# Optimization experiments

Measured on AMD Instinct MI355X. Metric: run time of the kernel, lower is better.

Reference implementation:

```python
import jax, jax.numpy as jnp
import numpy as np

N = 20000      # total nodes (100 graphs x 200 nodes)
B = 100        # batch_size
PER = 200      # nodes per graph (uniform) -> max_num_nodes
E = 320000     # edges (before self-loops)
F_IN = 32      # num_features
HEADS = 10
OUT = 128      # output_dim
NEG_SLOPE = 0.2  # PyG GATConv default


def setup_inputs() -> dict:
    key = jax.random.key(0)
    ks = jax.random.split(key, 14)
    feats = jax.random.normal(ks[0], (N, F_IN), jnp.float32)
    src = jax.random.randint(ks[1], (E,), 0, N)
    dst = jax.random.randint(ks[2], (E,), 0, N)
    edge_index = jnp.stack([src, dst]).astype(jnp.int32)
    graph_id = jnp.repeat(jnp.arange(B, dtype=jnp.int32), PER)
    batch_num_nodes = jnp.full((B,), PER, jnp.int32)
    s1 = 1.0 / np.sqrt(F_IN)
    s2 = 1.0 / np.sqrt(F_IN * HEADS)
    s3 = 1.0 / np.sqrt(OUT)
    return {
        "feats": feats,
        "edge_index": edge_index,
        "graph_id": graph_id,
        "batch_num_nodes": batch_num_nodes,
        # GATConv 1: in F_IN -> HEADS x F_IN, concat
        "W1": jax.random.normal(ks[3], (F_IN, HEADS * F_IN), jnp.float32) * s1,
        "a1_src": jax.random.normal(ks[4], (HEADS, F_IN), jnp.float32) * s1,
        "a1_dst": jax.random.normal(ks[5], (HEADS, F_IN), jnp.float32) * s1,
        "b1": jnp.zeros((HEADS * F_IN,), jnp.float32),
        "W2": jax.random.normal(ks[6], (HEADS * F_IN, OUT), jnp.float32) * s2,
        "a2_src": jax.random.normal(ks[7], (1, OUT), jnp.float32) * s3,
        "a2_dst": jax.random.normal(ks[8], (1, OUT), jnp.float32) * s3,
        "b2": jnp.zeros((OUT,), jnp.float32),
        # shared fc_g1
        "fc_w": jax.random.normal(ks[9], (OUT, OUT), jnp.float32) * s3,
        "fc_b": jnp.zeros((OUT,), jnp.float32),
    }


def gat_conv(x, src, dst, W, a_src, a_dst, bias, heads, out_dim):
    # x: [N, Fin]; src/dst already include self-loops (PyG default add_self_loops=True)
    n = x.shape[0]
    xw = (x @ W).reshape(n, heads, out_dim)                 # [N,H,F]
    s_src = jnp.einsum('nhf,hf->nh', xw, a_src)             # [N,H]
    s_dst = jnp.einsum('nhf,hf->nh', xw, a_dst)
    e = jax.nn.leaky_relu(s_src[src] + s_dst[dst], NEG_SLOPE)  # [E,H]
    # segment softmax over incoming edges of each destination node
    m = jax.ops.segment_max(e, dst, num_segments=n)         # [N,H]
    ex = jnp.exp(e - m[dst])
    denom = jax.ops.segment_sum(ex, dst, num_segments=n)    # [N,H]
    alpha = ex / jnp.maximum(denom[dst], 1e-16)             # [E,H]
    out = jax.ops.segment_sum(alpha[:, :, None] * xw[src], dst, num_segments=n)  # [N,H,F]
    return out.reshape(n, heads * out_dim) + bias


def reference(feats, edge_index, graph_id, batch_num_nodes,
              W1, a1_src, a1_dst, b1, W2, a2_src, a2_dst, b2, fc_w, fc_b):
    n = feats.shape[0]
    loops = jnp.arange(n, dtype=edge_index.dtype)
    src = jnp.concatenate([edge_index[0], loops])
    dst = jnp.concatenate([edge_index[1], loops])
    x = feats.astype(jnp.float32)
    # dropout layers are identity in eval mode
    x = jax.nn.elu(gat_conv(x, src, dst, W1, a1_src, a1_dst, b1, HEADS, F_IN))
    x = gat_conv(x, src, dst, W2, a2_src, a2_dst, b2, 1, OUT)
    x = jax.nn.relu(x)                                       # [N, OUT]
    # dgl_split: scatter node feats into [B, max_num_nodes, OUT] padded tensor
    cum = jnp.concatenate([jnp.zeros((1,), jnp.int32),
                           jnp.cumsum(batch_num_nodes).astype(jnp.int32)])
    idx = jnp.arange(n, dtype=jnp.int32) - cum[graph_id] + graph_id * PER
    padded = jnp.zeros((B * PER, OUT), x.dtype).at[idx].set(x).reshape(B, PER, OUT)
    out = jax.nn.relu(padded @ fc_w + fc_b)                  # [B, PER, OUT]
    # global max pool per graph, then shared fc_g1 + relu
    pooled = jax.ops.segment_max(x, graph_id, num_segments=B)  # [B, OUT]
    pooled = jax.nn.relu(pooled @ fc_w + fc_b)
    return (out, pooled)
```

## Files before the change

kernel.cpp:

```cpp
#include <hip/hip_runtime.h>

#define N_NODES 20000
#define N_EDGES 320000
#define ETOT    (N_EDGES + N_NODES)
#define HEADS   10
#define F_IN    32
#define C1      (HEADS * F_IN)
#define C2      128
#define NB      100
#define PER     200
#define CAP     96
#define HSTRIDE 328
#define X2STRIDE 136

typedef __attribute__((ext_vector_type(8))) short bf16x8;
typedef __attribute__((ext_vector_type(4))) float floatx4;
typedef _Float16 f16;
typedef _Float16 f16x2 __attribute__((ext_vector_type(2)));
typedef _Float16 f16x8 __attribute__((ext_vector_type(8)));

static __device__ __forceinline__ unsigned short f2bf(float f) {
    unsigned int u = __float_as_uint(f);
    unsigned int r = (u + 0x7fffu + ((u >> 16) & 1u)) >> 16;
    return (unsigned short)r;
}

#define CURZ_BLOCKS ((N_NODES + 255) / 256)
#define PLZ_BLOCKS  ((NB * C2 + 255) / 256)
#define W2P_BLOCKS  ((C1 * C2 + 255) / 256)
#define W1P_BLOCKS  ((HEADS * F_IN * F_IN + 255) / 256)
#define FCP_BLOCKS  ((C2 * C2 + 255) / 256)
#define F16_BLOCKS  ((N_NODES * F_IN / 4 + 255) / 256)
__global__ void prep_kernel(int* __restrict__ cursor, int* __restrict__ pooledi,
                            const float* __restrict__ W2, unsigned short* __restrict__ W2p,
                            const float* __restrict__ W1, unsigned short* __restrict__ W1p,
                            const float* __restrict__ fcw, f16* __restrict__ FCp,
                            const float* __restrict__ a1s, const float* __restrict__ a1d,
                            float* __restrict__ WAs, float* __restrict__ WAd,
                            const float* __restrict__ feats, f16* __restrict__ feats16) {
    unsigned int b = blockIdx.x;
    if (b < CURZ_BLOCKS) {
        int o = b * 256 + threadIdx.x;
        if (o < N_NODES) cursor[o] = 0;
        return;
    }
    b -= CURZ_BLOCKS;
    if (b < PLZ_BLOCKS) {
        int o = b * 256 + threadIdx.x;
        if (o < NB * C2) pooledi[o] = 0;
        return;
    }
    b -= PLZ_BLOCKS;
    if (b < W2P_BLOCKS) {
        int o = b * 256 + threadIdx.x;
        if (o >= C1 * C2) return;
        int j    = o & 7;
        int lane = (o >> 3) & 63;
        int ct   = (o >> 9) & 7;
        int kb   = o >> 12;
        int k = kb * 32 + (lane >> 4) * 8 + j;
        int n = ct * 16 + (lane & 15);
        W2p[o] = f2bf(W2[k * C2 + n]);
        return;
    }
    b -= W2P_BLOCKS;
    if (b < W1P_BLOCKS) {
        int o = b * 256 + threadIdx.x;
        if (o >= HEADS * F_IN * F_IN) return;
        int j    = o & 7;
        int lane = (o >> 3) & 63;
        int ct   = (o >> 9) & 1;
        int h    = o >> 10;
        int k = (lane >> 4) * 8 + j;
        int f = ct * 16 + (lane & 15);
        W1p[o] = f2bf(W1[k * C1 + h * 32 + f]);
        return;
    }
    b -= W1P_BLOCKS;
    if (b < FCP_BLOCKS) {
        int o = b * 256 + threadIdx.x;
        if (o >= C2 * C2) return;
        int j    = o & 7;
        int lane = (o >> 3) & 63;
        int ct   = (o >> 9) & 7;
        int kb   = o >> 12;
        int k = kb * 32 + (lane >> 4) * 8 + j;
        int n = ct * 16 + (lane & 15);
        FCp[o] = (f16)fcw[k * C2 + n];
        return;
    }
    b -= FCP_BLOCKS;
    if (b < F16_BLOCKS) {
        int o = b * 256 + threadIdx.x;
        if (o < N_NODES * F_IN / 4) {
            float4 v = ((const float4*)feats)[o];
            f16* d = feats16 + 4 * o;
            d[0] = (f16)v.x; d[1] = (f16)v.y; d[2] = (f16)v.z; d[3] = (f16)v.w;
        }
        return;
    }
    int t = threadIdx.x;
    for (int o = t; o < C1; o += 256) {
        int k = o & 31, h = o >> 5;
        float ss = 0.f, dd = 0.f;
#pragma unroll
        for (int f = 0; f < F_IN; f++) {
            float wv = W1[k * C1 + h * 32 + f];
            ss += wv * a1s[h * 32 + f];
            dd += wv * a1d[h * 32 + f];
        }
        WAs[k * HEADS + h] = ss;
        WAd[k * HEADS + h] = dd;
    }
}

#define SCAT_BLOCKS ((ETOT + 255) / 256)
__global__ __launch_bounds__(256) void scatter_score_kernel(
        const int* __restrict__ ei, int* __restrict__ cursor, int* __restrict__ csr_src,
        const float* __restrict__ feats, const float* __restrict__ WAs,
        const float* __restrict__ WAd, float* __restrict__ s_src,
        float* __restrict__ s_dst) {
    if (blockIdx.x < SCAT_BLOCKS) {
        int e = blockIdx.x * 256 + threadIdx.x;
        if (e >= ETOT) return;
        int s, d;
        if (e < N_EDGES) { s = ei[e]; d = ei[N_EDGES + e]; }
        else             { s = e - N_EDGES; d = s; }
        int pos = atomicAdd(&cursor[d], 1);
        csr_src[(size_t)d * CAP + pos] = s;
        return;
    }
    __shared__ __align__(16) float A[64 * F_IN];
    __shared__ float Ws[C1], Wd[C1];
    int t = threadIdx.x;
    int n0 = (blockIdx.x - SCAT_BLOCKS) * 64;
    int nrows = min(64, N_NODES - n0);
    if (nrows <= 0) return;
    for (int i = t; i < C1; i += 256) { Ws[i] = WAs[i]; Wd[i] = WAd[i]; }
    const float4* fs = (const float4*)(feats + (size_t)n0 * F_IN);
    float4* Af = (float4*)A;
    for (int i = t; i < nrows * 8; i += 256) Af[i] = fs[i];
    __syncthreads();
    for (int o = t; o < nrows * HEADS; o += 256) {
        int nl = o / HEADS, h = o - nl * HEADS;
        const float* ar = A + nl * F_IN;
        float ss = 0.f, dd = 0.f;
#pragma unroll
        for (int k = 0; k < F_IN; k++) {
            float av = ar[k];
            ss += av * Ws[k * HEADS + h];
            dd += av * Wd[k * HEADS + h];
        }
        s_src[(size_t)(n0 + nl) * HEADS + h] = ss;
        s_dst[(size_t)(n0 + nl) * HEADS + h] = dd;
    }
}

__global__ __launch_bounds__(256) void aggg1_kernel(
        const f16* __restrict__ feats16, const float* __restrict__ s_src,
        const float* __restrict__ s_dst, const int* __restrict__ deg_arr,
        const int* __restrict__ csr_src, unsigned short* __restrict__ gn) {
    __shared__ __align__(4) f16 shP[4][HEADS * 64];
    __shared__ __align__(8) int shS[4][64];
    int wslot = threadIdx.x >> 6;
    int n = blockIdx.x * 4 + wslot;
    int lane = threadIdx.x & 63;
    int k = lane & 31, half = lane >> 5;
    f16* P = shP[wslot];
    int* S = shS[wslot];
    const f16x2 ones = {(f16)1.f, (f16)1.f};

    int beg = n * CAP, deg = deg_arr[n];
    const float* sdp = s_dst + (size_t)n * HEADS;
    float sd[10];
#pragma unroll
    for (int q = 0; q < 5; q++) {
        float2 v = *(const float2*)(sdp + 2 * q);
        sd[2 * q] = v.x; sd[2 * q + 1] = v.y;
    }
    float g[10], la[10];
#pragma unroll
    for (int h = 0; h < 10; h++) { g[h] = 0.f; la[h] = 0.f; }

    for (int c0 = 0; c0 < deg; c0 += 64) {
        int dc = min(deg - c0, 64);
        bool act = lane < dc;
        int s_e = csr_src[beg + c0 + min(lane, dc - 1)];
        const float* ssp = s_src + (size_t)s_e * HEADS;
        float p[10];
#pragma unroll
        for (int q = 0; q < 5; q++) {
            float2 v = *(const float2*)(ssp + 2 * q);
            float e0 = v.x + sd[2 * q];
            float e1 = v.y + sd[2 * q + 1];
            e0 = (e0 >= 0.f) ? e0 : 0.2f * e0;
            e1 = (e1 >= 0.f) ? e1 : 0.2f * e1;
            p[2 * q]     = act ? __expf(e0) : 0.f;
            p[2 * q + 1] = act ? __expf(e1) : 0.f;
        }
        S[lane] = s_e;
#pragma unroll
        for (int h = 0; h < 10; h++) P[h * 64 + lane] = (f16)p[h];
        asm volatile("s_waitcnt lgkmcnt(0)" ::: "memory");

        int dcp = (dc + 3) & ~3;
        for (int i = 0; i < dcp; i += 4) {
            int e0 = i + half * 2;
            int2 ss2 = *(const int2*)&S[e0];
            f16x2 v;
            v.x = feats16[(size_t)ss2.x * F_IN + k];
            v.y = feats16[(size_t)ss2.y * F_IN + k];
#pragma unroll
            for (int h = 0; h < 10; h++) {
                f16x2 pp = *(const f16x2*)&P[h * 64 + e0];
                g[h]  = __builtin_amdgcn_fdot2(pp, v, g[h], false);
                la[h] = __builtin_amdgcn_fdot2(pp, ones, la[h], false);
            }
        }
        asm volatile("s_waitcnt lgkmcnt(0)" ::: "memory");
    }
#pragma unroll
    for (int h = 0; h < 10; h++) {
        g[h]  += __shfl_xor(g[h], 32);
        la[h] += __shfl_xor(la[h], 32);
    }
    if (half == 0) {
        unsigned short* gp = gn + (size_t)n * C1 + k;
#pragma unroll
        for (int h = 0; h < 10; h++)
            gp[h * 32] = f2bf(g[h] / fmaxf(la[h], 1e-16f));
    }
}

__global__ __launch_bounds__(256) void h1gemm2_kernel(
        const unsigned short* __restrict__ gn, const unsigned short* __restrict__ W1p,
        const float* __restrict__ b1, const unsigned short* __restrict__ W2p,
        const float* __restrict__ a_src, const float* __restrict__ a_dst,
        f16* __restrict__ xw2h, float* __restrict__ s_src2, float* __restrict__ s_dst2) {
    __shared__ unsigned short H[2][16 * HSTRIDE];
    __shared__ float redS[2][2][16], redD[2][2][16];
    int waveId = threadIdx.x >> 6;
    int tl = waveId >> 1;
    int w  = waveId & 1;
    int tile = blockIdx.x * 2 + tl;
    int lane = threadIdx.x & 63;
    int quad = lane >> 4, col = lane & 15;
    int row0 = tile * 16;

#pragma unroll
    for (int hh = 0; hh < 5; hh++) {
        int h = w * 5 + hh;
        bf16x8 a = *(const bf16x8*)(gn + (size_t)(row0 + col) * C1 + h * 32 + quad * 8);
        bf16x8 bA = ((const bf16x8*)W1p)[(h * 2 + 0) * 64 + lane];
        bf16x8 bB = ((const bf16x8*)W1p)[(h * 2 + 1) * 64 + lane];
        floatx4 z = {0.f, 0.f, 0.f, 0.f};
        floatx4 c0 = __builtin_amdgcn_mfma_f32_16x16x32_bf16(a, bA, z, 0, 0, 0);
        floatx4 c1 = __builtin_amdgcn_mfma_f32_16x16x32_bf16(a, bB, z, 0, 0, 0);
        float bias0 = b1[h * 32 + col];
        float bias1 = b1[h * 32 + 16 + col];
#pragma unroll
        for (int reg = 0; reg < 4; reg++) {
            int r = quad * 4 + reg;
            float o0 = c0[reg] + bias0;
            float o1 = c1[reg] + bias1;
            o0 = (o0 > 0.f) ? o0 : (__expf(o0) - 1.f);
            o1 = (o1 > 0.f) ? o1 : (__expf(o1) - 1.f);
            H[tl][r * HSTRIDE + h * 32 + col]      = f2bf(o0);
            H[tl][r * HSTRIDE + h * 32 + 16 + col] = f2bf(o1);
        }
    }
    __syncthreads();

    floatx4 acc[4];
#pragma unroll
    for (int c = 0; c < 4; c++) acc[c] = (floatx4){0.f, 0.f, 0.f, 0.f};
    const bf16x8* pb = (const bf16x8*)W2p;
#pragma unroll
    for (int kb = 0; kb < 10; kb++) {
        bf16x8 a = *(const bf16x8*)&H[tl][(lane & 15) * HSTRIDE + kb * 32 + quad * 8];
#pragma unroll
        for (int c = 0; c < 4; c++) {
            bf16x8 b = pb[(kb * 8 + (4 * w + c)) * 64 + lane];
            acc[c] = __builtin_amdgcn_mfma_f32_16x16x32_bf16(a, b, acc[c], 0, 0, 0);
        }
    }
    float asv[4], adv[4];
#pragma unroll
    for (int c = 0; c < 4; c++) {
        asv[c] = a_src[(4 * w + c) * 16 + col];
        adv[c] = a_dst[(4 * w + c) * 16 + col];
    }
#pragma unroll
    for (int reg = 0; reg < 4; reg++) {
        int row = row0 + quad * 4 + reg;
        float vs = 0.f, vd = 0.f;
#pragma unroll
        for (int c = 0; c < 4; c++) {
            float v = acc[c][reg];
            xw2h[(size_t)row * C2 + (4 * w + c) * 16 + col] = (f16)v;
            vs += v * asv[c];
            vd += v * adv[c];
        }
#pragma unroll
        for (int off = 8; off >= 1; off >>= 1) {
            vs += __shfl_xor(vs, off);
            vd += __shfl_xor(vd, off);
        }
        if (col == 0) { redS[tl][w][quad * 4 + reg] = vs; redD[tl][w][quad * 4 + reg] = vd; }
    }
    __syncthreads();
    if (w == 0) {
        if (lane < 16)
            s_src2[row0 + lane] = redS[tl][0][lane] + redS[tl][1][lane];
        else if (lane < 32)
            s_dst2[row0 + lane - 16] = redD[tl][0][lane - 16] + redD[tl][1][lane - 16];
    }
}

__global__ __launch_bounds__(256) void agg2fc_kernel(
        const f16* __restrict__ xw2h, const float* __restrict__ s_src2,
        const float* __restrict__ s_dst2, const int* __restrict__ deg_arr,
        const int* __restrict__ csr_src, const float* __restrict__ b2,
        const f16* __restrict__ FCp, const float* __restrict__ fcb,
        float* __restrict__ out, int* __restrict__ pooledi) {
    __shared__ __align__(8) int2 shE[4][64];
    __shared__ __align__(16) f16 X[16 * X2STRIDE];
    int wslot = threadIdx.x >> 6;
    int lane = threadIdx.x & 63;
    int tile = blockIdx.x;
    int row0 = tile * 16;
    int2* E = shE[wslot];

#pragma unroll
    for (int rep = 0; rep < 4; rep++) {
        int r = wslot * 4 + rep;
        int n = row0 + r;
        int beg = n * CAP, deg = deg_arr[n];
        float sd = s_dst2[n];
        float l = 0.f, a0 = 0.f, a1 = 0.f;

        for (int c0 = 0; c0 < deg; c0 += 64) {
            int dc = min(deg - c0, 64);
            bool act = lane < dc;
            int s_e = csr_src[beg + c0 + min(lane, dc - 1)];
            float e = s_src2[s_e] + sd;
            e = (e >= 0.f) ? e : 0.2f * e;
            float p = act ? __expf(e) : 0.f;
            float su = p;
#pragma unroll
            for (int off = 32; off >= 1; off >>= 1) su += __shfl_xor(su, off);
            l += su;

            E[lane] = make_int2(s_e, __float_as_int(p));
            asm volatile("s_waitcnt lgkmcnt(0)" ::: "memory");

            int dcr = (dc + 3) & ~3;
            for (int i = 0; i < dcr; i += 4) {
                int2 e0 = E[i + 0], e1 = E[i + 1], e2 = E[i + 2], e3 = E[i + 3];
                f16x2 v0 = *(const f16x2*)(xw2h + (size_t)e0.x * C2 + 2 * lane);
                f16x2 v1 = *(const f16x2*)(xw2h + (size_t)e1.x * C2 + 2 * lane);
                f16x2 v2 = *(const f16x2*)(xw2h + (size_t)e2.x * C2 + 2 * lane);
                f16x2 v3 = *(const f16x2*)(xw2h + (size_t)e3.x * C2 + 2 * lane);
                float p0 = __int_as_float(e0.y), p1 = __int_as_float(e1.y);
                float p2 = __int_as_float(e2.y), p3 = __int_as_float(e3.y);
                a0 += p0 * (float)v0.x + p1 * (float)v1.x + p2 * (float)v2.x + p3 * (float)v3.x;
                a1 += p0 * (float)v0.y + p1 * (float)v1.y + p2 * (float)v2.y + p3 * (float)v3.y;
            }
            asm volatile("s_waitcnt lgkmcnt(0)" ::: "memory");
        }

        float linv = 1.f / fmaxf(l, 1e-16f);
        float2 bb = *(const float2*)(b2 + 2 * lane);
        f16x2 o;
        o.x = (f16)fmaxf(a0 * linv + bb.x, 0.f);
        o.y = (f16)fmaxf(a1 * linv + bb.y, 0.f);
        *(f16x2*)&X[r * X2STRIDE + 2 * lane] = o;
    }
    __syncthreads();

    int quad = lane >> 4, col = lane & 15;
    floatx4 acc[2];
    acc[0] = (floatx4){0.f, 0.f, 0.f, 0.f};
    acc[1] = (floatx4){0.f, 0.f, 0.f, 0.f};
    const f16x8* pb = (const f16x8*)FCp;
#pragma unroll
    for (int kb = 0; kb < 4; kb++) {
        f16x8 a = *(const f16x8*)&X[(lane & 15) * X2STRIDE + kb * 32 + quad * 8];
#pragma unroll
        for (int c = 0; c < 2; c++) {
            int ct = wslot * 2 + c;
            f16x8 b = pb[(kb * 8 + ct) * 64 + lane];
            acc[c] = __builtin_amdgcn_mfma_f32_16x16x32_f16(a, b, acc[c], 0, 0, 0);
        }
    }
#pragma unroll
    for (int c = 0; c < 2; c++) {
        int ct = wslot * 2 + c;
        float bias = fcb[ct * 16 + col];
#pragma unroll
        for (int reg = 0; reg < 4; reg++) {
            int row = row0 + quad * 4 + reg;
            out[(size_t)row * C2 + ct * 16 + col] = fmaxf(acc[c][reg] + bias, 0.f);
        }
    }

    if (threadIdx.x < C2) {
        int c = threadIdx.x;
        int gA = row0 / PER;
        int gB = (row0 + 15) / PER;
        float mA = 0.f, mB = 0.f;
#pragma unroll
        for (int r = 0; r < 16; r++) {
            float v = (float)X[r * X2STRIDE + c];
            if ((row0 + r) / PER == gA) mA = fmaxf(mA, v);
            else                        mB = fmaxf(mB, v);
        }
        atomicMax(&pooledi[gA * C2 + c], __float_as_int(mA));
        if (gB != gA) atomicMax(&pooledi[gB * C2 + c], __float_as_int(mB));
    }
}

__global__ void poolfc_kernel(const int* __restrict__ pooledi, const float* __restrict__ fcw,
                              const float* __restrict__ fcb, float* __restrict__ outp) {
    __shared__ float mx[C2];
    int g = blockIdx.x, t = threadIdx.x;
    mx[t] = __int_as_float(pooledi[g * C2 + t]);
    __syncthreads();
    float acc = 0.f;
    for (int k = 0; k < C2; k++) acc += mx[k] * fcw[k * C2 + t];
    outp[g * C2 + t] = fmaxf(acc + fcb[t], 0.f);
}

extern "C" void kernel_launch(void* const* d_in, const int* in_sizes, int n_in,
                              void* d_out, int out_size, void* d_ws, size_t ws_size,
                              hipStream_t stream) {
    const float* feats = (const float*)d_in[0];
    const int*   ei    = (const int*)d_in[1];
    const float* W1  = (const float*)d_in[4];
    const float* a1s = (const float*)d_in[5];
    const float* a1d = (const float*)d_in[6];
    const float* b1  = (const float*)d_in[7];
    const float* W2  = (const float*)d_in[8];
    const float* a2s = (const float*)d_in[9];
    const float* a2d = (const float*)d_in[10];
    const float* b2  = (const float*)d_in[11];
    const float* fcw = (const float*)d_in[12];
    const float* fcb = (const float*)d_in[13];

    float* out_main = (float*)d_out;
    float* out_pool = (float*)d_out + (size_t)N_NODES * C2;

    char* p = (char*)d_ws;
    auto alloc = [&](size_t bytes) {
        char* r = p;
        p += (bytes + 255) & ~(size_t)255;
        return r;
    };
    unsigned short* gn   = (unsigned short*)alloc(sizeof(short) * (size_t)N_NODES * C1);
    unsigned short* W2p  = (unsigned short*)alloc(sizeof(short) * C1 * C2);
    unsigned short* W1p  = (unsigned short*)alloc(sizeof(short) * HEADS * F_IN * F_IN);
    f16*   FCp     = (f16*)alloc(sizeof(f16) * C2 * C2);
    f16*   feats16 = (f16*)alloc(sizeof(f16) * (size_t)N_NODES * F_IN);
    f16*   xw2h    = (f16*)alloc(sizeof(f16) * (size_t)N_NODES * C2);
    float* WAs    = (float*)alloc(sizeof(float) * C1);
    float* WAd    = (float*)alloc(sizeof(float) * C1);
    float* s1s    = (float*)alloc(sizeof(float) * N_NODES * HEADS);
    float* s1d    = (float*)alloc(sizeof(float) * N_NODES * HEADS);
    float* s2s    = (float*)alloc(sizeof(float) * N_NODES);
    float* s2d    = (float*)alloc(sizeof(float) * N_NODES);
    int* cursor   = (int*)alloc(sizeof(int) * N_NODES);
    int* pooledi  = (int*)alloc(sizeof(int) * NB * C2);
    int* csr_src  = (int*)alloc(sizeof(int) * N_NODES * CAP);

    prep_kernel<<<CURZ_BLOCKS + PLZ_BLOCKS + W2P_BLOCKS + W1P_BLOCKS + FCP_BLOCKS + F16_BLOCKS + 1,
                  256, 0, stream>>>(
        cursor, pooledi, W2, W2p, W1, W1p, fcw, FCp, a1s, a1d, WAs, WAd, feats, feats16);
    scatter_score_kernel<<<SCAT_BLOCKS + (N_NODES + 63) / 64, 256, 0, stream>>>(
        ei, cursor, csr_src, feats, WAs, WAd, s1s, s1d);

    aggg1_kernel<<<5000, 256, 0, stream>>>(feats16, s1s, s1d, cursor, csr_src, gn);
    h1gemm2_kernel<<<625, 256, 0, stream>>>(gn, W1p, b1, W2p, a2s, a2d, xw2h, s2s, s2d);
    agg2fc_kernel<<<1250, 256, 0, stream>>>(xw2h, s2s, s2d, cursor, csr_src, b2,
                                            FCp, fcb, out_main, pooledi);
    poolfc_kernel<<<NB, C2, 0, stream>>>(pooledi, fcw, fcb, out_pool);
}
```

Measured before the change: 167.3 us.

## Fuse layer-1 aggregation with layer-1 projection and layer-2 GEMM in one kernel

Merges the layer-1 edge aggregation kernel and the following W1/ELU/W2 GEMM kernel into one 512-thread block per 16-node tile. Aggregated features now stay in shared memory instead of making a round trip through a global bf16 buffer, and one launch is removed. The agg2fc kernel also moves to 8 waves per 16-row tile, with each wave owning one 16-column output slice. The cost is lower per-block GEMM parallelism, since waves 0-1 handle two heads while the rest handle one. Larger blocks and higher LDS use per block may also reduce occupancy.

```diff
diff --git a/kernel.cpp b/kernel.cpp
--- a/kernel.cpp
+++ b/kernel.cpp
@@ -156,101 +156,96 @@
     }
 }
 
-__global__ __launch_bounds__(256) void aggg1_kernel(
+__global__ __launch_bounds__(512) void aggh1g2_kernel(
         const f16* __restrict__ feats16, const float* __restrict__ s_src,
         const float* __restrict__ s_dst, const int* __restrict__ deg_arr,
-        const int* __restrict__ csr_src, unsigned short* __restrict__ gn) {
-    __shared__ __align__(4) f16 shP[4][HEADS * 64];
-    __shared__ __align__(8) int shS[4][64];
-    int wslot = threadIdx.x >> 6;
-    int n = blockIdx.x * 4 + wslot;
+        const int* __restrict__ csr_src,
+        const unsigned short* __restrict__ W1p, const float* __restrict__ b1,
+        const unsigned short* __restrict__ W2p,
+        const float* __restrict__ a_src, const float* __restrict__ a_dst,
+        f16* __restrict__ xw2h, float* __restrict__ s_src2, float* __restrict__ s_dst2) {
+    __shared__ __align__(4) f16 shP[8][HEADS * 64];
+    __shared__ __align__(8) int shS[8][64];
+    __shared__ __align__(16) unsigned short GT[16 * HSTRIDE];
+    __shared__ __align__(16) unsigned short H[16 * HSTRIDE];
+    __shared__ float redS[8][16], redD[8][16];
+    int w = threadIdx.x >> 6;
     int lane = threadIdx.x & 63;
     int k = lane & 31, half = lane >> 5;
-    f16* P = shP[wslot];
-    int* S = shS[wslot];
+    int row0 = blockIdx.x * 16;
+    f16* P = shP[w];
+    int* S = shS[w];
     const f16x2 ones = {(f16)1.f, (f16)1.f};
 
-    int beg = n * CAP, deg = deg_arr[n];
-    const float* sdp = s_dst + (size_t)n * HEADS;
-    float sd[10];
-#pragma unroll
-    for (int q = 0; q < 5; q++) {
-        float2 v = *(const float2*)(sdp + 2 * q);
-        sd[2 * q] = v.x; sd[2 * q + 1] = v.y;
-    }
-    float g[10], la[10];
-#pragma unroll
-    for (int h = 0; h < 10; h++) { g[h] = 0.f; la[h] = 0.f; }
-
-    for (int c0 = 0; c0 < deg; c0 += 64) {
-        int dc = min(deg - c0, 64);
-        bool act = lane < dc;
-        int s_e = csr_src[beg + c0 + min(lane, dc - 1)];
-        const float* ssp = s_src + (size_t)s_e * HEADS;
-        float p[10];
+#pragma unroll
+    for (int rep = 0; rep < 2; rep++) {
+        int r = w * 2 + rep;
+        int n = row0 + r;
+        int beg = n * CAP, deg = deg_arr[n];
+        const float* sdp = s_dst + (size_t)n * HEADS;
+        float sd[10];
 #pragma unroll
         for (int q = 0; q < 5; q++) {
-            float2 v = *(const float2*)(ssp + 2 * q);
-            float e0 = v.x + sd[2 * q];
-            float e1 = v.y + sd[2 * q + 1];
-            e0 = (e0 >= 0.f) ? e0 : 0.2f * e0;
-            e1 = (e1 >= 0.f) ? e1 : 0.2f * e1;
-            p[2 * q]     = act ? __expf(e0) : 0.f;
-            p[2 * q + 1] = act ? __expf(e1) : 0.f;
-        }
-        S[lane] = s_e;
-#pragma unroll
-        for (int h = 0; h < 10; h++) P[h * 64 + lane] = (f16)p[h];
-        asm volatile("s_waitcnt lgkmcnt(0)" ::: "memory");
-
-        int dcp = (dc + 3) & ~3;
-        for (int i = 0; i < dcp; i += 4) {
-            int e0 = i + half * 2;
-            int2 ss2 = *(const int2*)&S[e0];
-            f16x2 v;
-            v.x = feats16[(size_t)ss2.x * F_IN + k];
-            v.y = feats16[(size_t)ss2.y * F_IN + k];
-#pragma unroll
-            for (int h = 0; h < 10; h++) {
-                f16x2 pp = *(const f16x2*)&P[h * 64 + e0];
-                g[h]  = __builtin_amdgcn_fdot2(pp, v, g[h], false);
-                la[h] = __builtin_amdgcn_fdot2(pp, ones, la[h], false);
+            float2 v = *(const float2*)(sdp + 2 * q);
+            sd[2 * q] = v.x; sd[2 * q + 1] = v.y;
+        }
+        float g[10], la[10];
+#pragma unroll
+        for (int h = 0; h < 10; h++) { g[h] = 0.f; la[h] = 0.f; }
+
+        for (int c0 = 0; c0 < deg; c0 += 64) {
+            int dc = min(deg - c0, 64);
+            bool act = lane < dc;
+            int s_e = csr_src[beg + c0 + min(lane, dc - 1)];
+            const float* ssp = s_src + (size_t)s_e * HEADS;
+            float p[10];
+#pragma unroll
+            for (int q = 0; q < 5; q++) {
+                float2 v = *(const float2*)(ssp + 2 * q);
+                float e0 = v.x + sd[2 * q];
+                float e1 = v.y + sd[2 * q + 1];
+                e0 = (e0 >= 0.f) ? e0 : 0.2f * e0;
+                e1 = (e1 >= 0.f) ? e1 : 0.2f * e1;
+                p[2 * q]     = act ? __expf(e0) : 0.f;
+                p[2 * q + 1] = act ? __expf(e1) : 0.f;
             }
-        }
-        asm volatile("s_waitcnt lgkmcnt(0)" ::: "memory");
-    }
-#pragma unroll
-    for (int h = 0; h < 10; h++) {
-        g[h]  += __shfl_xor(g[h], 32);
-        la[h] += __shfl_xor(la[h], 32);
-    }
-    if (half == 0) {
-        unsigned short* gp = gn + (size_t)n * C1 + k;
-#pragma unroll
-        for (int h = 0; h < 10; h++)
-            gp[h * 32] = f2bf(g[h] / fmaxf(la[h], 1e-16f));
-    }
-}
-
-__global__ __launch_bounds__(256) void h1gemm2_kernel(
-        const unsigned short* __restrict__ gn, const unsigned short* __restrict__ W1p,
-        const float* __restrict__ b1, const unsigned short* __restrict__ W2p,
-        const float* __restrict__ a_src, const float* __restrict__ a_dst,
-        f16* __restrict__ xw2h, float* __restrict__ s_src2, float* __restrict__ s_dst2) {
-    __shared__ unsigned short H[2][16 * HSTRIDE];
-    __shared__ float redS[2][2][16], redD[2][2][16];
-    int waveId = threadIdx.x >> 6;
-    int tl = waveId >> 1;
-    int w  = waveId & 1;
-    int tile = blockIdx.x * 2 + tl;
-    int lane = threadIdx.x & 63;
+            S[lane] = s_e;
+#pragma unroll
+            for (int h = 0; h < 10; h++) P[h * 64 + lane] = (f16)p[h];
+            asm volatile("s_waitcnt lgkmcnt(0)" ::: "memory");
+
+            int dcp = (dc + 3) & ~3;
+            for (int i = 0; i < dcp; i += 4) {
+                int e0 = i + half * 2;
+                int2 ss2 = *(const int2*)&S[e0];
+                f16x2 v;
+                v.x = feats16[(size_t)ss2.x * F_IN + k];
+                v.y = feats16[(size_t)ss2.y * F_IN + k];
+#pragma unroll
+                for (int h = 0; h < 10; h++) {
+                    f16x2 pp = *(const f16x2*)&P[h * 64 + e0];
+                    g[h]  = __builtin_amdgcn_fdot2(pp, v, g[h], false);
+                    la[h] = __builtin_amdgcn_fdot2(pp, ones, la[h], false);
+                }
+            }
+            asm volatile("s_waitcnt lgkmcnt(0)" ::: "memory");
+        }
+#pragma unroll
+        for (int h = 0; h < 10; h++) {
+            g[h]  += __shfl_xor(g[h], 32);
+            la[h] += __shfl_xor(la[h], 32);
+        }
+        if (half == 0) {
+#pragma unroll
+            for (int h = 0; h < 10; h++)
+                GT[r * HSTRIDE + h * 32 + k] = f2bf(g[h] / fmaxf(la[h], 1e-16f));
+        }
+    }
+    __syncthreads();
+
     int quad = lane >> 4, col = lane & 15;
-    int row0 = tile * 16;
-
-#pragma unroll
-    for (int hh = 0; hh < 5; hh++) {
-        int h = w * 5 + hh;
-        bf16x8 a = *(const bf16x8*)(gn + (size_t)(row0 + col) * C1 + h * 32 + quad * 8);
+    for (int h = w; h < 10; h += 8) {
+        bf16x8 a = *(const bf16x8*)&GT[col * HSTRIDE + h * 32 + quad * 8];
         bf16x8 bA = ((const bf16x8*)W1p)[(h * 2 + 0) * 64 + lane];
         bf16x8 bB = ((const bf16x8*)W1p)[(h * 2 + 1) * 64 + lane];
         floatx4 z = {0.f, 0.f, 0.f, 0.f};
@@ -265,75 +260,60 @@
             float o1 = c1[reg] + bias1;
             o0 = (o0 > 0.f) ? o0 : (__expf(o0) - 1.f);
             o1 = (o1 > 0.f) ? o1 : (__expf(o1) - 1.f);
-            H[tl][r * HSTRIDE + h * 32 + col]      = f2bf(o0);
-            H[tl][r * HSTRIDE + h * 32 + 16 + col] = f2bf(o1);
-        }
-    }
-    __syncthreads();
-
-    floatx4 acc[4];
-#pragma unroll
-    for (int c = 0; c < 4; c++) acc[c] = (floatx4){0.f, 0.f, 0.f, 0.f};
+            H[r * HSTRIDE + h * 32 + col]      = f2bf(o0);
+            H[r * HSTRIDE + h * 32 + 16 + col] = f2bf(o1);
+        }
+    }
+    __syncthreads();
+
+    floatx4 acc = {0.f, 0.f, 0.f, 0.f};
     const bf16x8* pb = (const bf16x8*)W2p;
 #pragma unroll
     for (int kb = 0; kb < 10; kb++) {
-        bf16x8 a = *(const bf16x8*)&H[tl][(lane & 15) * HSTRIDE + kb * 32 + quad * 8];
-#pragma unroll
-        for (int c = 0; c < 4; c++) {
-            bf16x8 b = pb[(kb * 8 + (4 * w + c)) * 64 + lane];
-            acc[c] = __builtin_amdgcn_mfma_f32_16x16x32_bf16(a, b, acc[c], 0, 0, 0);
-        }
-    }
-    float asv[4], adv[4];
-#pragma unroll
-    for (int c = 0; c < 4; c++) {
-        asv[c] = a_src[(4 * w + c) * 16 + col];
-        adv[c] = a_dst[(4 * w + c) * 16 + col];
-    }
+        bf16x8 a = *(const bf16x8*)&H[(lane & 15) * HSTRIDE + kb * 32 + quad * 8];
+        bf16x8 b = pb[(kb * 8 + w) * 64 + lane];
+        acc = __builtin_amdgcn_mfma_f32_16x16x32_bf16(a, b, acc, 0, 0, 0);
+    }
+    float as = a_src[w * 16 + col], ad = a_dst[w * 16 + col];
 #pragma unroll
     for (int reg = 0; reg < 4; reg++) {
         int row = row0 + quad * 4 + reg;
-        float vs = 0.f, vd = 0.f;
-#pragma unroll
-        for (int c = 0; c < 4; c++) {
-            float v = acc[c][reg];
-            xw2h[(size_t)row * C2 + (4 * w + c) * 16 + col] = (f16)v;
-            vs += v * asv[c];
-            vd += v * adv[c];
-        }
+        float v = acc[reg];
+        xw2h[(size_t)row * C2 + w * 16 + col] = (f16)v;
+        float vs = v * as, vd = v * ad;
 #pragma unroll
         for (int off = 8; off >= 1; off >>= 1) {
             vs += __shfl_xor(vs, off);
             vd += __shfl_xor(vd, off);
         }
-        if (col == 0) { redS[tl][w][quad * 4 + reg] = vs; redD[tl][w][quad * 4 + reg] = vd; }
-    }
-    __syncthreads();
-    if (w == 0) {
-        if (lane < 16)
-            s_src2[row0 + lane] = redS[tl][0][lane] + redS[tl][1][lane];
-        else if (lane < 32)
-            s_dst2[row0 + lane - 16] = redD[tl][0][lane - 16] + redD[tl][1][lane - 16];
-    }
-}
-
-__global__ __launch_bounds__(256) void agg2fc_kernel(
+        if (col == 0) { redS[w][quad * 4 + reg] = vs; redD[w][quad * 4 + reg] = vd; }
+    }
+    __syncthreads();
+    if (threadIdx.x < 16) {
+        float s = 0.f, d = 0.f;
+#pragma unroll
+        for (int ww = 0; ww < 8; ww++) { s += redS[ww][threadIdx.x]; d += redD[ww][threadIdx.x]; }
+        s_src2[row0 + threadIdx.x] = s;
+        s_dst2[row0 + threadIdx.x] = d;
+    }
+}
+
+__global__ __launch_bounds__(512) void agg2fc_kernel(
         const f16* __restrict__ xw2h, const float* __restrict__ s_src2,
         const float* __restrict__ s_dst2, const int* __restrict__ deg_arr,
         const int* __restrict__ csr_src, const float* __restrict__ b2,
         const f16* __restrict__ FCp, const float* __restrict__ fcb,
         float* __restrict__ out, int* __restrict__ pooledi) {
-    __shared__ __align__(8) int2 shE[4][64];
+    __shared__ __align__(8) int2 shE[8][64];
     __shared__ __align__(16) f16 X[16 * X2STRIDE];
-    int wslot = threadIdx.x >> 6;
+    int w = threadIdx.x >> 6;
     int lane = threadIdx.x & 63;
-    int tile = blockIdx.x;
-    int row0 = tile * 16;
-    int2* E = shE[wslot];
-
-#pragma unroll
-    for (int rep = 0; rep < 4; rep++) {
-        int r = wslot * 4 + rep;
+    int row0 = blockIdx.x * 16;
+    int2* E = shE[w];
+
+#pragma unroll
+    for (int rep = 0; rep < 2; rep++) {
+        int r = w * 2 + rep;
         int n = row0 + r;
         int beg = n * CAP, deg = deg_arr[n];
         float sd = s_dst2[n];
@@ -379,29 +359,19 @@
     __syncthreads();
 
     int quad = lane >> 4, col = lane & 15;
-    floatx4 acc[2];
-    acc[0] = (floatx4){0.f, 0.f, 0.f, 0.f};
-    acc[1] = (floatx4){0.f, 0.f, 0.f, 0.f};
+    floatx4 acc = {0.f, 0.f, 0.f, 0.f};
     const f16x8* pb = (const f16x8*)FCp;
 #pragma unroll
     for (int kb = 0; kb < 4; kb++) {
         f16x8 a = *(const f16x8*)&X[(lane & 15) * X2STRIDE + kb * 32 + quad * 8];
-#pragma unroll
-        for (int c = 0; c < 2; c++) {
-            int ct = wslot * 2 + c;
-            f16x8 b = pb[(kb * 8 + ct) * 64 + lane];
-            acc[c] = __builtin_amdgcn_mfma_f32_16x16x32_f16(a, b, acc[c], 0, 0, 0);
-        }
-    }
-#pragma unroll
-    for (int c = 0; c < 2; c++) {
-        int ct = wslot * 2 + c;
-        float bias = fcb[ct * 16 + col];
-#pragma unroll
-        for (int reg = 0; reg < 4; reg++) {
-            int row = row0 + quad * 4 + reg;
-            out[(size_t)row * C2 + ct * 16 + col] = fmaxf(acc[c][reg] + bias, 0.f);
-        }
+        f16x8 b = pb[(kb * 8 + w) * 64 + lane];
+        acc = __builtin_amdgcn_mfma_f32_16x16x32_f16(a, b, acc, 0, 0, 0);
+    }
+    float bias = fcb[w * 16 + col];
+#pragma unroll
+    for (int reg = 0; reg < 4; reg++) {
+        int row = row0 + quad * 4 + reg;
+        out[(size_t)row * C2 + w * 16 + col] = fmaxf(acc[reg] + bias, 0.f);
     }
 
     if (threadIdx.x < C2) {
@@ -456,7 +426,6 @@
         p += (bytes + 255) & ~(size_t)255;
         return r;
     };
-    unsigned short* gn   = (unsigned short*)alloc(sizeof(short) * (size_t)N_NODES * C1);
     unsigned short* W2p  = (unsigned short*)alloc(sizeof(short) * C1 * C2);
     unsigned short* W1p  = (unsigned short*)alloc(sizeof(short) * HEADS * F_IN * F_IN);
     f16*   FCp     = (f16*)alloc(sizeof(f16) * C2 * C2);
@@ -478,9 +447,9 @@
     scatter_score_kernel<<<SCAT_BLOCKS + (N_NODES + 63) / 64, 256, 0, stream>>>(
         ei, cursor, csr_src, feats, WAs, WAd, s1s, s1d);
 
-    aggg1_kernel<<<5000, 256, 0, stream>>>(feats16, s1s, s1d, cursor, csr_src, gn);
-    h1gemm2_kernel<<<625, 256, 0, stream>>>(gn, W1p, b1, W2p, a2s, a2d, xw2h, s2s, s2d);
-    agg2fc_kernel<<<1250, 256, 0, stream>>>(xw2h, s2s, s2d, cursor, csr_src, b2,
+    aggh1g2_kernel<<<1250, 512, 0, stream>>>(feats16, s1s, s1d, cursor, csr_src,
+                                             W1p, b1, W2p, a2s, a2d, xw2h, s2s, s2d);
+    agg2fc_kernel<<<1250, 512, 0, stream>>>(xw2h, s2s, s2d, cursor, csr_src, b2,
                                             FCp, fcb, out_main, pooledi);
     poolfc_kernel<<<NB, C2, 0, stream>>>(pooledi, fcw, fcb, out_pool);
 }
```

Result: no change. 169.4 us (+1.2%).

## Merge prep and scatter kernels, fold pool-FC into last agg2fc block

Applied to the files above, without the earlier changes.

Replaces the zeroing blocks with a single hipMemsetAsync and merges the prep and scatter/score kernels into one launch. Each score block now recomputes the W1·a projections itself instead of reading them from a separate buffer. The pooled FC is done by the last-finishing agg2fc block, found with a done-counter atomic, which removes the final poolfc launch. This trades launch overhead for serial tail work: one block runs all 100 graph FCs sequentially, and the projection is computed redundantly in every score block.

```diff
diff --git a/kernel.cpp b/kernel.cpp
--- a/kernel.cpp
+++ b/kernel.cpp
@@ -25,32 +25,70 @@
     return (unsigned short)r;
 }
 
-#define CURZ_BLOCKS ((N_NODES + 255) / 256)
-#define PLZ_BLOCKS  ((NB * C2 + 255) / 256)
-#define W2P_BLOCKS  ((C1 * C2 + 255) / 256)
-#define W1P_BLOCKS  ((HEADS * F_IN * F_IN + 255) / 256)
-#define FCP_BLOCKS  ((C2 * C2 + 255) / 256)
-#define F16_BLOCKS  ((N_NODES * F_IN / 4 + 255) / 256)
-__global__ void prep_kernel(int* __restrict__ cursor, int* __restrict__ pooledi,
-                            const float* __restrict__ W2, unsigned short* __restrict__ W2p,
-                            const float* __restrict__ W1, unsigned short* __restrict__ W1p,
-                            const float* __restrict__ fcw, f16* __restrict__ FCp,
-                            const float* __restrict__ a1s, const float* __restrict__ a1d,
-                            float* __restrict__ WAs, float* __restrict__ WAd,
-                            const float* __restrict__ feats, f16* __restrict__ feats16) {
+#define SCAT_BLOCKS  ((ETOT + 255) / 256)
+#define SCORE_BLOCKS ((N_NODES + 63) / 64)
+#define W2P_BLOCKS   ((C1 * C2 + 255) / 256)
+#define W1P_BLOCKS   ((HEADS * F_IN * F_IN + 255) / 256)
+#define FCP_BLOCKS   ((C2 * C2 + 255) / 256)
+#define F16_BLOCKS   ((N_NODES * F_IN / 4 + 255) / 256)
+__global__ __launch_bounds__(256) void mega_prep_kernel(
+        const int* __restrict__ ei, int* __restrict__ cursor, int* __restrict__ csr_src,
+        const float* __restrict__ feats, f16* __restrict__ feats16,
+        const float* __restrict__ W1, unsigned short* __restrict__ W1p,
+        const float* __restrict__ W2, unsigned short* __restrict__ W2p,
+        const float* __restrict__ fcw, f16* __restrict__ FCp,
+        const float* __restrict__ a1s, const float* __restrict__ a1d,
+        float* __restrict__ s_src, float* __restrict__ s_dst) {
     unsigned int b = blockIdx.x;
-    if (b < CURZ_BLOCKS) {
-        int o = b * 256 + threadIdx.x;
-        if (o < N_NODES) cursor[o] = 0;
+    if (b < SCAT_BLOCKS) {
+        int e = b * 256 + threadIdx.x;
+        if (e >= ETOT) return;
+        int s, d;
+        if (e < N_EDGES) { s = ei[e]; d = ei[N_EDGES + e]; }
+        else             { s = e - N_EDGES; d = s; }
+        int pos = atomicAdd(&cursor[d], 1);
+        csr_src[(size_t)d * CAP + pos] = s;
         return;
     }
-    b -= CURZ_BLOCKS;
-    if (b < PLZ_BLOCKS) {
-        int o = b * 256 + threadIdx.x;
-        if (o < NB * C2) pooledi[o] = 0;
+    b -= SCAT_BLOCKS;
+    if (b < SCORE_BLOCKS) {
+        __shared__ __align__(16) float A[64 * F_IN];
+        __shared__ float Ws[C1], Wd[C1];
+        int t = threadIdx.x;
+        for (int o = t; o < C1; o += 256) {
+            int k = o & 31, h = o >> 5;
+            float ss = 0.f, dd = 0.f;
+#pragma unroll
+            for (int f = 0; f < F_IN; f++) {
+                float wv = W1[k * C1 + h * 32 + f];
+                ss += wv * a1s[h * 32 + f];
+                dd += wv * a1d[h * 32 + f];
+            }
+            Ws[k * HEADS + h] = ss;
+            Wd[k * HEADS + h] = dd;
+        }
+        int n0 = b * 64;
+        int nrows = min(64, N_NODES - n0);
+        const float4* fs = (const float4*)(feats + (size_t)n0 * F_IN);
+        float4* Af = (float4*)A;
+        for (int i = t; i < nrows * 8; i += 256) Af[i] = fs[i];
+        __syncthreads();
+        for (int o = t; o < nrows * HEADS; o += 256) {
+            int nl = o / HEADS, h = o - nl * HEADS;
+            const float* ar = A + nl * F_IN;
+            float ss = 0.f, dd = 0.f;
+#pragma unroll
+            for (int k = 0; k < F_IN; k++) {
+                float av = ar[k];
+                ss += av * Ws[k * HEADS + h];
+                dd += av * Wd[k * HEADS + h];
+            }
+            s_src[(size_t)(n0 + nl) * HEADS + h] = ss;
+            s_dst[(size_t)(n0 + nl) * HEADS + h] = dd;
+        }
         return;
     }
-    b -= PLZ_BLOCKS;
+    b -= SCORE_BLOCKS;
     if (b < W2P_BLOCKS) {
         int o = b * 256 + threadIdx.x;
         if (o >= C1 * C2) return;
@@ -90,69 +128,13 @@
         return;
     }
     b -= FCP_BLOCKS;
-    if (b < F16_BLOCKS) {
+    {
         int o = b * 256 + threadIdx.x;
         if (o < N_NODES * F_IN / 4) {
             float4 v = ((const float4*)feats)[o];
             f16* d = feats16 + 4 * o;
             d[0] = (f16)v.x; d[1] = (f16)v.y; d[2] = (f16)v.z; d[3] = (f16)v.w;
         }
-        return;
-    }
-    int t = threadIdx.x;
-    for (int o = t; o < C1; o += 256) {
-        int k = o & 31, h = o >> 5;
-        float ss = 0.f, dd = 0.f;
-#pragma unroll
-        for (int f = 0; f < F_IN; f++) {
-            float wv = W1[k * C1 + h * 32 + f];
-            ss += wv * a1s[h * 32 + f];
-            dd += wv * a1d[h * 32 + f];
-        }
-        WAs[k * HEADS + h] = ss;
-        WAd[k * HEADS + h] = dd;
-    }
-}
-
-#define SCAT_BLOCKS ((ETOT + 255) / 256)
-__global__ __launch_bounds__(256) void scatter_score_kernel(
-        const int* __restrict__ ei, int* __restrict__ cursor, int* __restrict__ csr_src,
-        const float* __restrict__ feats, const float* __restrict__ WAs,
-        const float* __restrict__ WAd, float* __restrict__ s_src,
-        float* __restrict__ s_dst) {
-    if (blockIdx.x < SCAT_BLOCKS) {
-        int e = blockIdx.x * 256 + threadIdx.x;
-        if (e >= ETOT) return;
-        int s, d;
-        if (e < N_EDGES) { s = ei[e]; d = ei[N_EDGES + e]; }
-        else             { s = e - N_EDGES; d = s; }
-        int pos = atomicAdd(&cursor[d], 1);
-        csr_src[(size_t)d * CAP + pos] = s;
-        return;
-    }
-    __shared__ __align__(16) float A[64 * F_IN];
-    __shared__ float Ws[C1], Wd[C1];
-    int t = threadIdx.x;
-    int n0 = (blockIdx.x - SCAT_BLOCKS) * 64;
-    int nrows = min(64, N_NODES - n0);
-    if (nrows <= 0) return;
-    for (int i = t; i < C1; i += 256) { Ws[i] = WAs[i]; Wd[i] = WAd[i]; }
-    const float4* fs = (const float4*)(feats + (size_t)n0 * F_IN);
-    float4* Af = (float4*)A;
-    for (int i = t; i < nrows * 8; i += 256) Af[i] = fs[i];
-    __syncthreads();
-    for (int o = t; o < nrows * HEADS; o += 256) {
-        int nl = o / HEADS, h = o - nl * HEADS;
-        const float* ar = A + nl * F_IN;
-        float ss = 0.f, dd = 0.f;
-#pragma unroll
-        for (int k = 0; k < F_IN; k++) {
-            float av = ar[k];
-            ss += av * Ws[k * HEADS + h];
-            dd += av * Wd[k * HEADS + h];
-        }
-        s_src[(size_t)(n0 + nl) * HEADS + h] = ss;
-        s_dst[(size_t)(n0 + nl) * HEADS + h] = dd;
     }
 }
 
@@ -321,14 +303,17 @@
         const f16* __restrict__ xw2h, const float* __restrict__ s_src2,
         const float* __restrict__ s_dst2, const int* __restrict__ deg_arr,
         const int* __restrict__ csr_src, const float* __restrict__ b2,
-        const f16* __restrict__ FCp, const float* __restrict__ fcb,
-        float* __restrict__ out, int* __restrict__ pooledi) {
+        const f16* __restrict__ FCp, const float* __restrict__ fcw,
+        const float* __restrict__ fcb, float* __restrict__ out,
+        int* __restrict__ pooledi, int* __restrict__ donecnt,
+        float* __restrict__ outp) {
     __shared__ __align__(8) int2 shE[4][64];
     __shared__ __align__(16) f16 X[16 * X2STRIDE];
+    __shared__ float mx[C2];
+    __shared__ int isLast;
     int wslot = threadIdx.x >> 6;
     int lane = threadIdx.x & 63;
-    int tile = blockIdx.x;
-    int row0 = tile * 16;
+    int row0 = blockIdx.x * 16;
     int2* E = shE[wslot];
 
 #pragma unroll
@@ -418,17 +403,26 @@
         atomicMax(&pooledi[gA * C2 + c], __float_as_int(mA));
         if (gB != gA) atomicMax(&pooledi[gB * C2 + c], __float_as_int(mB));
     }
-}
-
-__global__ void poolfc_kernel(const int* __restrict__ pooledi, const float* __restrict__ fcw,
-                              const float* __restrict__ fcb, float* __restrict__ outp) {
-    __shared__ float mx[C2];
-    int g = blockIdx.x, t = threadIdx.x;
-    mx[t] = __int_as_float(pooledi[g * C2 + t]);
+
+    __threadfence();
+    if (threadIdx.x == 0) {
+        int v = atomicAdd(donecnt, 1);
+        isLast = (v == (int)gridDim.x - 1);
+    }
     __syncthreads();
-    float acc = 0.f;
-    for (int k = 0; k < C2; k++) acc += mx[k] * fcw[k * C2 + t];
-    outp[g * C2 + t] = fmaxf(acc + fcb[t], 0.f);
+    if (!isLast) return;
+    for (int g = 0; g < NB; g++) {
+        if (threadIdx.x < C2)
+            mx[threadIdx.x] = __int_as_float(atomicAdd(&pooledi[g * C2 + threadIdx.x], 0));
+        __syncthreads();
+        if (threadIdx.x < C2) {
+            int t = threadIdx.x;
+            float acc2 = 0.f;
+            for (int k = 0; k < C2; k++) acc2 += mx[k] * fcw[k * C2 + t];
+            outp[g * C2 + t] = fmaxf(acc2 + fcb[t], 0.f);
+        }
+        __syncthreads();
+    }
 }
 
 extern "C" void kernel_launch(void* const* d_in, const int* in_sizes, int n_in,
@@ -462,25 +456,26 @@
     f16*   FCp     = (f16*)alloc(sizeof(f16) * C2 * C2);
     f16*   feats16 = (f16*)alloc(sizeof(f16) * (size_t)N_NODES * F_IN);
     f16*   xw2h    = (f16*)alloc(sizeof(f16) * (size_t)N_NODES * C2);
-    float* WAs    = (float*)alloc(sizeof(float) * C1);
-    float* WAd    = (float*)alloc(sizeof(float) * C1);
     float* s1s    = (float*)alloc(sizeof(float) * N_NODES * HEADS);
     float* s1d    = (float*)alloc(sizeof(float) * N_NODES * HEADS);
     float* s2s    = (float*)alloc(sizeof(float) * N_NODES);
     float* s2d    = (float*)alloc(sizeof(float) * N_NODES);
-    int* cursor   = (int*)alloc(sizeof(int) * N_NODES);
-    int* pooledi  = (int*)alloc(sizeof(int) * NB * C2);
-    int* csr_src  = (int*)alloc(sizeof(int) * N_NODES * CAP);
-
-    prep_kernel<<<CURZ_BLOCKS + PLZ_BLOCKS + W2P_BLOCKS + W1P_BLOCKS + FCP_BLOCKS + F16_BLOCKS + 1,
-                  256, 0, stream>>>(
-        cursor, pooledi, W2, W2p, W1, W1p, fcw, FCp, a1s, a1d, WAs, WAd, feats, feats16);
-    scatter_score_kernel<<<SCAT_BLOCKS + (N_NODES + 63) / 64, 256, 0, stream>>>(
-        ei, cursor, csr_src, feats, WAs, WAd, s1s, s1d);
+    const int NZ = N_NODES + NB * C2 + 64;
+    int* zeros   = (int*)alloc(sizeof(int) * NZ);
+    int* cursor  = zeros;
+    int* pooledi = zeros + N_NODES;
+    int* donecnt = zeros + N_NODES + NB * C2;
+    int* csr_src = (int*)alloc(sizeof(int) * N_NODES * CAP);
+
+    hipMemsetAsync(zeros, 0, sizeof(int) * NZ, stream);
+
+    mega_prep_kernel<<<SCAT_BLOCKS + SCORE_BLOCKS + W2P_BLOCKS + W1P_BLOCKS + FCP_BLOCKS + F16_BLOCKS,
+                       256, 0, stream>>>(
+        ei, cursor, csr_src, feats, feats16, W1, W1p, W2, W2p, fcw, FCp,
+        a1s, a1d, s1s, s1d);
 
     aggg1_kernel<<<5000, 256, 0, stream>>>(feats16, s1s, s1d, cursor, csr_src, gn);
     h1gemm2_kernel<<<625, 256, 0, stream>>>(gn, W1p, b1, W2p, a2s, a2d, xw2h, s2s, s2d);
     agg2fc_kernel<<<1250, 256, 0, stream>>>(xw2h, s2s, s2d, cursor, csr_src, b2,
-                                            FCp, fcb, out_main, pooledi);
-    poolfc_kernel<<<NB, C2, 0, stream>>>(pooledi, fcw, fcb, out_pool);
-}
+                                            FCp, fcw, fcb, out_main, pooledi, donecnt, out_pool);
+}
```

After: 456.1 us. 2.73x slower.
